# Performance work log

Measured on AMD Instinct MI355X. Metric: run time of the kernel, lower is better.

Reference implementation:

```python
import jax, jax.numpy as jnp
import numpy as np

N = 8192
K = 64
EPS = 1e-7
BN_EPS = 1e-5


def _norm(x):
    return jnp.sqrt(jnp.sum(x * x, axis=-1, keepdims=True))


def _bn(x, gamma, beta):
    # BatchNorm2d in training mode (batch statistics, biased variance)
    mu = jnp.mean(x, axis=(0, 2, 3), keepdims=True)
    var = jnp.mean((x - mu) ** 2, axis=(0, 2, 3), keepdims=True)
    return gamma.reshape(1, -1, 1, 1) * (x - mu) / jnp.sqrt(var + BN_EPS) + beta.reshape(1, -1, 1, 1)


def _conv1x1(x, w, b):
    # 1x1 conv == per-pixel linear: x [B,C,H,W], w [O,C]
    return jnp.einsum('bchw,oc->bohw', x, w) + b.reshape(1, -1, 1, 1)


def setup_inputs() -> dict:
    key = jax.random.key(0)
    ks = jax.random.split(key, 24)
    d = {}
    d['points'] = jax.random.normal(ks[0], (1, N, 3), jnp.float32)
    # graph_conv weights (torch code re-draws these every forward; here fixed params)
    lim0 = float(np.sqrt(6.0 / (4 + 64)))
    d['gw0'] = jax.random.uniform(ks[1], (4, 64), jnp.float32, -lim0, lim0)
    lim = float(np.sqrt(6.0 / (64 + 64)))
    for i in range(1, 5):
        d[f'gw{i}'] = jax.random.uniform(ks[1 + i], (64, 64), jnp.float32, -lim, lim)
    # mlp_1: 4->64->128, mlp_2: 192->256->1024 (1x1 convs + BN)
    d['c1w'] = jax.random.normal(ks[6], (64, 4), jnp.float32) * 0.1
    d['c1b'] = jnp.zeros((64,), jnp.float32)
    d['bn1g'] = jnp.ones((64,), jnp.float32)
    d['bn1b'] = jnp.zeros((64,), jnp.float32)
    d['c2w'] = jax.random.normal(ks[7], (128, 64), jnp.float32) * 0.1
    d['c2b'] = jnp.zeros((128,), jnp.float32)
    d['bn2g'] = jnp.ones((128,), jnp.float32)
    d['bn2b'] = jnp.zeros((128,), jnp.float32)
    d['c3w'] = jax.random.normal(ks[8], (256, 192), jnp.float32) * 0.05
    d['c3b'] = jnp.zeros((256,), jnp.float32)
    d['bn3g'] = jnp.ones((256,), jnp.float32)
    d['bn3b'] = jnp.zeros((256,), jnp.float32)
    d['c4w'] = jax.random.normal(ks[9], (1024, 256), jnp.float32) * 0.05
    d['c4b'] = jnp.zeros((1024,), jnp.float32)
    d['bn4g'] = jnp.ones((1024,), jnp.float32)
    d['bn4b'] = jnp.zeros((1024,), jnp.float32)
    return d


def _knn_search(points, k):
    # pairwise squared distances via ||a||^2 - 2ab + ||b||^2
    r = jnp.sum(points * points, axis=-1, keepdims=True)          # [1,N,1]
    dis = r - 2.0 * jnp.einsum('bnd,bmd->bnm', points, points) + jnp.swapaxes(r, 1, 2)
    _, idx = jax.lax.top_k(-dis, k)                                # [1,N,K]
    knn_pts = jax.vmap(lambda p, i: p[i])(points, idx)             # [1,N,K,3]
    return knn_pts


def _proj_knn(knn_pts):
    b, n, k, _ = knn_pts.shape
    pc = knn_pts - knn_pts[:, :, :1, :]                            # center on first neighbor (self)
    vn = jnp.sqrt(jnp.sum(pc * pc, axis=-1))                       # [1,N,K]
    id1 = jnp.argmax(vn, axis=-1)                                  # farthest neighbor
    a1 = jnp.take_along_axis(pc, jnp.broadcast_to(id1[:, :, None, None], (b, n, 1, 3)), axis=2)[:, :, 0, :]
    a1 = a1 / (_norm(a1) + EPS)
    a2 = jnp.mean(pc, axis=2)
    a2 = a2 / (_norm(a2) + EPS)
    a3 = a1 + 1.5 * a2
    a3 = a3 / (_norm(a3) + EPS)
    den = _norm(pc) + EPS                                          # [1,N,K,1]
    f1 = jnp.sum(pc * a1[:, :, None, :], axis=-1, keepdims=True) / den
    f2 = jnp.sum(pc * a2[:, :, None, :], axis=-1, keepdims=True) / den
    f3 = jnp.sum(pc * a3[:, :, None, :], axis=-1, keepdims=True) / den
    return jnp.concatenate([f1, f2, f3, vn[..., None]], axis=-1)   # [1,N,K,4]


def _proj_points(points):
    b, n, _ = points.shape
    vn = jnp.sqrt(jnp.sum(points * points, axis=-1))               # [1,N]
    i1 = jnp.argmax(vn, axis=-1)
    i2 = jnp.argmin(vn, axis=-1)
    a1 = jnp.take_along_axis(points, jnp.broadcast_to(i1[:, None, None], (b, 1, 3)), axis=1)[:, 0, :]
    a1 = a1 / (_norm(a1) + EPS)
    a2 = jnp.take_along_axis(points, jnp.broadcast_to(i2[:, None, None], (b, 1, 3)), axis=1)[:, 0, :]
    a2 = a2 / (_norm(a2) + EPS)
    a3 = a1 + 1.5 * a2
    a3 = a3 / (_norm(a3) + EPS)
    den = _norm(points) + EPS                                      # [1,N,1]
    f1 = jnp.sum(points * a1[:, None, :], axis=-1, keepdims=True) / den
    f2 = jnp.sum(points * a2[:, None, :], axis=-1, keepdims=True) / den
    f3 = jnp.sum(points * a3[:, None, :], axis=-1, keepdims=True) / den
    return jnp.concatenate([f1, f2, f3, vn[..., None]], axis=-1)   # [1,N,4]


def reference(points, gw0, gw1, gw2, gw3, gw4,
              c1w, c1b, bn1g, bn1b, c2w, c2b, bn2g, bn2b,
              c3w, c3b, bn3g, bn3b, c4w, c4b, bn4g, bn4b):
    n = points.shape[1]
    # upper branch: KNN -> rotation-invariant local feats -> 5-layer MLP -> max over K
    knn_pts = _knn_search(points, K)
    feat_up = _proj_knn(knn_pts)                                   # [1,N,K,4]
    x = feat_up.reshape(-1, 4)
    for w in (gw0, gw1, gw2, gw3, gw4):
        x = jax.nn.relu(x @ w)
    x = x.reshape(1, n, K, 64)
    emb_up = jnp.max(x, axis=2, keepdims=True)                     # [1,N,1,64]
    emb_up = emb_up.reshape(1, 64, n, 1)                           # raw view (reshape), as in torch
    # lower branch: global rotation-invariant feats -> mlp_1
    feat_down = _proj_points(points)                               # [1,N,4]
    emb_down = feat_down.reshape(1, 4, n, 1)                       # raw view (reshape), as in torch
    h = jax.nn.relu(_bn(_conv1x1(emb_down, c1w, c1b), bn1g, bn1b))
    h = jax.nn.relu(_bn(_conv1x1(h, c2w, c2b), bn2g, bn2b))        # [1,128,N,1]
    emb = jnp.concatenate([emb_up, h], axis=1)                     # [1,192,N,1]
    out = jax.nn.relu(_bn(_conv1x1(emb, c3w, c3b), bn3g, bn3b))
    out = jax.nn.relu(_bn(_conv1x1(out, c4w, c4b), bn4g, bn4b))    # [1,1024,N,1]
    return out
```

## Files before the change

kernel.cpp:

```cpp
#include <hip/hip_runtime.h>
#include <hip/hip_bf16.h>

#define NPTS 8192
#define KNN 64
#define EPSF 1e-7f

#define OFF_P4      0
#define OFF_STATS   32768
#define OFF_PART    36012
#define OFF_FEATDN  36864
#define OFF_WT1     69632
#define OFF_GWT     69888
#define OFF_BW2     79104
#define OFF_BW3     83200
#define OFF_BW4     107776
#define OFF_XB3V    238848
#define OFF_Y2      2860288
#define OFF_Y3      3908864
#define OFF_FEATUP  6006016

typedef __bf16 bf16x8 __attribute__((ext_vector_type(8)));
typedef float  f32x4  __attribute__((ext_vector_type(4)));

__device__ __forceinline__ unsigned f2u(float f) {
    unsigned u = __float_as_uint(f);
    return ((int)u >= 0) ? (u | 0x80000000u) : ~u;
}
__device__ __forceinline__ float key_to_f(unsigned long long k) {
    unsigned v = (unsigned)(k >> 32);
    unsigned ob = (v & 0x80000000u) ? (v ^ 0x80000000u) : ~v;
    return __uint_as_float(ob);
}
__device__ __forceinline__ unsigned short f2bf(float x) {
    union { __bf16 h; unsigned short s; } u;
    u.h = (__bf16)x;
    return u.s;
}
__device__ __forceinline__ unsigned packbf2(float lo, float hi) {
    return (unsigned)f2bf(lo) | ((unsigned)f2bf(hi) << 16);
}
__device__ __forceinline__ unsigned long long u64min(unsigned long long a, unsigned long long b){ return a < b ? a : b; }
__device__ __forceinline__ unsigned long long u64max(unsigned long long a, unsigned long long b){ return a < b ? b : a; }

__device__ __forceinline__ unsigned long long sort_merge(
    unsigned long long key, unsigned long long cur, int lane)
{
    #pragma unroll
    for (int k = 2; k <= 64; k <<= 1) {
        #pragma unroll
        for (int j = k >> 1; j > 0; j >>= 1) {
            unsigned long long o = __shfl_xor(key, j);
            bool up = ((lane & k) == 0);
            bool lower = ((lane & j) == 0);
            key = (lower == up) ? u64min(key, o) : u64max(key, o);
        }
    }
    unsigned long long rev = __shfl(key, 63 - lane);
    unsigned long long m = u64min(cur, rev);
    #pragma unroll
    for (int j = 32; j > 0; j >>= 1) {
        unsigned long long o = __shfl_xor(m, j);
        m = ((lane & j) == 0) ? u64min(m, o) : u64max(m, o);
    }
    return m;
}

__global__ __launch_bounds__(256) void prepwt_kernel(
    const float* __restrict__ points,
    const float* __restrict__ c1w, const float* __restrict__ c2w,
    const float* __restrict__ c3w, const float* __restrict__ c4w,
    const float* __restrict__ gw0, const float* __restrict__ gw1,
    const float* __restrict__ gw2, const float* __restrict__ gw3,
    const float* __restrict__ gw4,
    float* __restrict__ ws)
{
    const int t = blockIdx.x * 256 + threadIdx.x;
    const int T = 256 * 256;
    for (int m = t; m < 2944; m += T) ws[OFF_STATS + m] = 0.f;
    for (int m = t; m < 64*4; m += T) { int o = m >> 2, c = m & 3; ws[OFF_WT1 + c*64 + o] = c1w[m]; }

    unsigned short* bw2 = (unsigned short*)(ws + OFF_BW2);
    for (int m = t; m < 128*64; m += T)   bw2[m] = f2bf(c2w[m]);
    unsigned short* bw3 = (unsigned short*)(ws + OFF_BW3);
    for (int m = t; m < 256*192; m += T)  bw3[m] = f2bf(c3w[m]);
    unsigned short* bw4 = (unsigned short*)(ws + OFF_BW4);
    for (int m = t; m < 1024*256; m += T) bw4[m] = f2bf(c4w[m]);

    unsigned short* gwt = (unsigned short*)(ws + OFF_GWT);
    for (int m = t; m < 2048; m += T) {
        int o = m >> 5, i = m & 31;
        gwt[m] = (i < 4) ? f2bf(gw0[i*64 + o]) : (unsigned short)0;
    }
    const float* gsrc[4] = {gw1, gw2, gw3, gw4};
    for (int l = 0; l < 4; ++l) {
        const float* g = gsrc[l];
        unsigned short* dst = gwt + 2048 + l*4096;
        for (int m = t; m < 4096; m += T) { int o = m >> 6, i = m & 63; dst[m] = f2bf(g[i*64 + o]); }
    }

    if (blockIdx.x < 32) {
        const int n = blockIdx.x * 256 + threadIdx.x;
        float x = points[3*n+0], y = points[3*n+1], z = points[3*n+2];
        float rr = x*x + y*y + z*z;
        ((float4*)(ws + OFF_P4))[n] = make_float4(x, y, z, rr);
        float vn = sqrtf(rr);
        unsigned b = __float_as_uint(vn);
        unsigned long long mxk = ((unsigned long long)b << 32) | (unsigned long long)(0xFFFFFFFFu - (unsigned)n);
        unsigned long long mnk = ((unsigned long long)b << 32) | (unsigned long long)(unsigned)n;
        for (int j = 32; j > 0; j >>= 1) {
            mxk = u64max(mxk, __shfl_xor(mxk, j));
            mnk = u64min(mnk, __shfl_xor(mnk, j));
        }
        __shared__ unsigned long long smx[4], smn[4];
        int wid = threadIdx.x >> 6;
        if ((threadIdx.x & 63) == 0) { smx[wid] = mxk; smn[wid] = mnk; }
        __syncthreads();
        if (threadIdx.x == 0) {
            unsigned long long MX = 0ull, MN = ~0ull;
            for (int i = 0; i < 4; ++i) { MX = u64max(MX, smx[i]); MN = u64min(MN, smn[i]); }
            unsigned long long* parts = (unsigned long long*)(ws + OFF_PART);
            parts[2*blockIdx.x + 0] = MX;
            parts[2*blockIdx.x + 1] = MN;
        }
    }
}

__global__ __launch_bounds__(512) void knn_feat_kernel(
    const float4* __restrict__ p4, float4* __restrict__ feat_up,
    float* __restrict__ ws)
{
    __shared__ __align__(16) float4 scand[2048];
    __shared__ unsigned long long queue[8][128];
    const int lane = threadIdx.x & 63;
    const int wid  = threadIdx.x >> 6;
    const int q = blockIdx.x * 8 + wid;

    const float4 qa = p4[q];
    unsigned long long cur = ~0ull;
    float ke = __builtin_inff();
    int qc = 0;
    unsigned long long* Q = queue[wid];

    for (int base = 0; base < NPTS; base += 2048) {
        __syncthreads();
        for (int t = threadIdx.x; t < 2048; t += 512) scand[t] = p4[base + t];
        __syncthreads();
        #pragma unroll 2
        for (int sub = 0; sub < 2048; sub += 128) {
            float4 cd0 = scand[sub + lane];
            float4 cd1 = scand[sub + 64 + lane];
            float dot0 = fmaf(qa.x, cd0.x, fmaf(qa.y, cd0.y, qa.z * cd0.z));
            float dot1 = fmaf(qa.x, cd1.x, fmaf(qa.y, cd1.y, qa.z * cd1.z));
            float e0 = fmaf(-2.f, dot0, cd0.w);
            float e1 = fmaf(-2.f, dot1, cd1.w);
            bool p0 = e0 < ke;
            bool p1 = e1 < ke;
            unsigned long long m0 = __ballot(p0);
            unsigned long long m1 = __ballot(p1);
            if (m0) {
                int prefix = __builtin_amdgcn_mbcnt_hi((unsigned)(m0 >> 32),
                              __builtin_amdgcn_mbcnt_lo((unsigned)m0, 0));
                if (p0) Q[qc + prefix] = ((unsigned long long)f2u(e0) << 32)
                                       | (unsigned long long)(unsigned)(base + sub + lane);
                qc += __popcll(m0);
                if (qc >= 64) {
                    qc -= 64;
                    cur = sort_merge(Q[qc + lane], cur, lane);
                    ke = key_to_f(__shfl(cur, 63));
                }
            }
            if (m1) {
                int prefix = __builtin_amdgcn_mbcnt_hi((unsigned)(m1 >> 32),
                              __builtin_amdgcn_mbcnt_lo((unsigned)m1, 0));
                if (p1) Q[qc + prefix] = ((unsigned long long)f2u(e1) << 32)
                                       | (unsigned long long)(unsigned)(base + sub + 64 + lane);
                qc += __popcll(m1);
                if (qc >= 64) {
                    qc -= 64;
                    cur = sort_merge(Q[qc + lane], cur, lane);
                    ke = key_to_f(__shfl(cur, 63));
                }
            }
        }
    }
    cur = sort_merge((lane < qc) ? Q[lane] : ~0ull, cur, lane);

    int nidx = (int)(unsigned)(cur & 0xFFFFFFFFu);
    float4 np = p4[nidx];
    float ox = __shfl(np.x, 0), oy = __shfl(np.y, 0), oz = __shfl(np.z, 0);
    float pcx = np.x - ox, pcy = np.y - oy, pcz = np.z - oz;
    float vn = sqrtf(pcx*pcx + pcy*pcy + pcz*pcz);

    unsigned long long ak = ((unsigned long long)__float_as_uint(vn) << 32)
                          | (unsigned long long)(unsigned)(63 - lane);
    for (int s = 32; s > 0; s >>= 1) ak = u64max(ak, __shfl_xor(ak, s));
    int id1 = 63 - (int)(unsigned)(ak & 0xFFFFFFFFu);

    float a1x = __shfl(pcx, id1), a1y = __shfl(pcy, id1), a1z = __shfl(pcz, id1);
    float n1 = sqrtf(a1x*a1x + a1y*a1y + a1z*a1z) + EPSF;
    a1x /= n1; a1y /= n1; a1z /= n1;

    float sx = pcx, sy = pcy, sz = pcz;
    for (int s = 32; s > 0; s >>= 1) {
        sx += __shfl_xor(sx, s); sy += __shfl_xor(sy, s); sz += __shfl_xor(sz, s);
    }
    float a2x = sx * (1.f/64.f), a2y = sy * (1.f/64.f), a2z = sz * (1.f/64.f);
    float n2 = sqrtf(a2x*a2x + a2y*a2y + a2z*a2z) + EPSF;
    a2x /= n2; a2y /= n2; a2z /= n2;

    float a3x = a1x + 1.5f*a2x, a3y = a1y + 1.5f*a2y, a3z = a1z + 1.5f*a2z;
    float n3 = sqrtf(a3x*a3x + a3y*a3y + a3z*a3z) + EPSF;
    a3x /= n3; a3y /= n3; a3z /= n3;

    float den = vn + EPSF;
    float f1 = (pcx*a1x + pcy*a1y + pcz*a1z) / den;
    float f2 = (pcx*a2x + pcy*a2y + pcz*a2z) / den;
    float f3 = (pcx*a3x + pcy*a3y + pcz*a3z) / den;
    feat_up[q*64 + lane] = make_float4(f1, f2, f3, vn);

    {
        const unsigned long long* parts = (const unsigned long long*)(ws + OFF_PART);
        unsigned long long mxk = (lane < 32) ? parts[2*lane + 0] : 0ull;
        unsigned long long mnk = (lane < 32) ? parts[2*lane + 1] : ~0ull;
        for (int s = 32; s > 0; s >>= 1) {
            mxk = u64max(mxk, __shfl_xor(mxk, s));
            mnk = u64min(mnk, __shfl_xor(mnk, s));
        }
        if (lane == 0) {
            int i1 = (int)(0xFFFFFFFFu - (unsigned)(mxk & 0xFFFFFFFFu));
            int i2 = (int)(unsigned)(mnk & 0xFFFFFFFFu);
            float4 p1 = p4[i1];
            float4 p2 = p4[i2];
            float w1 = sqrtf(p1.x*p1.x + p1.y*p1.y + p1.z*p1.z) + EPSF;
            float b1x = p1.x/w1, b1y = p1.y/w1, b1z = p1.z/w1;
            float w2 = sqrtf(p2.x*p2.x + p2.y*p2.y + p2.z*p2.z) + EPSF;
            float b2x = p2.x/w2, b2y = p2.y/w2, b2z = p2.z/w2;
            float b3x = b1x + 1.5f*b2x, b3y = b1y + 1.5f*b2y, b3z = b1z + 1.5f*b2z;
            float w3 = sqrtf(b3x*b3x + b3y*b3y + b3z*b3z) + EPSF;
            b3x /= w3; b3y /= w3; b3z /= w3;
            float vq = sqrtf(qa.w);
            float dq = vq + EPSF;
            float g1 = (qa.x*b1x + qa.y*b1y + qa.z*b1z) / dq;
            float g2 = (qa.x*b2x + qa.y*b2y + qa.z*b2z) / dq;
            float g3 = (qa.x*b3x + qa.y*b3y + qa.z*b3z) / dq;
            ((float4*)(ws + OFF_FEATDN))[q] = make_float4(g1, g2, g3, vq);
        }
    }
}

#define BROW 72
__global__ __launch_bounds__(256) void mlp_kernel(
    const float4* __restrict__ feat_up,
    const unsigned short* __restrict__ gwt,
    unsigned short* __restrict__ xb3v,
    const float* __restrict__ c1b,
    float* __restrict__ ws)
{
    __shared__ __align__(16) unsigned short Blds[4][64 * BROW];
    const int lane = threadIdx.x & 63;
    const int wid  = threadIdx.x >> 6;
    const int q = blockIdx.x * 4 + wid;
    const int c = lane & 15, g = lane >> 4;
    unsigned short* B = Blds[wid];

    {
        float4 f = feat_up[q*64 + lane];
        uint2 p0;
        p0.x = packbf2(f.x, f.y);
        p0.y = packbf2(f.z, f.w);
        *(uint2*)&B[lane*BROW] = p0;
        *(uint2*)&B[lane*BROW + 4] = make_uint2(0, 0);
        uint4 z4 = make_uint4(0, 0, 0, 0);
        *(uint4*)&B[lane*BROW + 8]  = z4;
        *(uint4*)&B[lane*BROW + 16] = z4;
        *(uint4*)&B[lane*BROW + 24] = z4;
    }

    const unsigned short* Wl[5] = {gwt, gwt + 2048, gwt + 6144, gwt + 10240, gwt + 14336};
    f32x4 acc[4][4];

    for (int layer = 0; layer < 5; ++layer) {
        const int wstride = (layer == 0) ? 32 : 64;
        const int nks = (layer == 0) ? 1 : 2;
        #pragma unroll
        for (int mb = 0; mb < 4; ++mb)
            #pragma unroll
            for (int nb = 0; nb < 4; ++nb)
                acc[mb][nb] = (f32x4){0.f, 0.f, 0.f, 0.f};

        for (int ks = 0; ks < nks; ++ks) {
            bf16x8 af[4], bf[4];
            #pragma unroll
            for (int mb = 0; mb < 4; ++mb)
                af[mb] = *(const bf16x8*)(Wl[layer] + (mb*16 + c)*wstride + ks*32 + g*8);
            #pragma unroll
            for (int nb = 0; nb < 4; ++nb)
                bf[nb] = *(const bf16x8*)&B[(nb*16 + c)*BROW + ks*32 + g*8];
            #pragma unroll
            for (int mb = 0; mb < 4; ++mb)
                #pragma unroll
                for (int nb = 0; nb < 4; ++nb)
                    acc[mb][nb] = __builtin_amdgcn_mfma_f32_16x16x32_bf16(af[mb], bf[nb], acc[mb][nb], 0, 0, 0);
        }

        if (layer < 4) {
            #pragma unroll
            for (int mb = 0; mb < 4; ++mb) {
                #pragma unroll
                for (int nb = 0; nb < 4; ++nb) {
                    f32x4 a = acc[mb][nb];
                    uint2 pw;
                    pw.x = packbf2(fmaxf(a[0], 0.f), fmaxf(a[1], 0.f));
                    pw.y = packbf2(fmaxf(a[2], 0.f), fmaxf(a[3], 0.f));
                    *(uint2*)&B[(nb*16 + c)*BROW + mb*16 + g*4] = pw;
                }
            }
        }
    }

    const int cc = q >> 7;
    const int pbase = (q & 127) << 6;
    #pragma unroll
    for (int mb = 0; mb < 4; ++mb) {
        float v[4];
        #pragma unroll
        for (int r = 0; r < 4; ++r)
            v[r] = fmaxf(fmaxf(fmaxf(acc[mb][0][r], acc[mb][1][r]),
                               fmaxf(acc[mb][2][r], acc[mb][3][r])), 0.f);
        #pragma unroll
        for (int mask = 1; mask <= 8; mask <<= 1)
            #pragma unroll
            for (int r = 0; r < 4; ++r)
                v[r] = fmaxf(v[r], __shfl_xor(v[r], mask));
        if (c == 0) {
            #pragma unroll
            for (int r = 0; r < 4; ++r) {
                const int f = mb*16 + g*4 + r;
                xb3v[(size_t)(pbase + f) * 64 + cc] = f2bf(v[r]);
            }
        }
    }

    if (blockIdx.x < 64) {
        __syncthreads();
        float* sps  = (float*)&Blds[0][0];
        float* spss = sps + 128;
        const int tid = threadIdx.x;
        const int bx = blockIdx.x & 31, by = blockIdx.x >> 5;
        const int p  = bx * 256 + tid;
        const int o0 = by * 32;
        const float* fdn = ws + OFF_FEATDN;
        const float* wt1 = ws + OFF_WT1;
        float* s1 = ws + OFF_STATS;
        float xv0 = fdn[p], xv1 = fdn[8192 + p], xv2 = fdn[16384 + p], xv3 = fdn[24576 + p];
        float accc[32];
        #pragma unroll
        for (int u = 0; u < 32; ++u) accc[u] = c1b[o0 + u];
        #pragma unroll
        for (int u = 0; u < 32; ++u) accc[u] = fmaf(xv0, wt1[0*64 + o0 + u], accc[u]);
        #pragma unroll
        for (int u = 0; u < 32; ++u) accc[u] = fmaf(xv1, wt1[1*64 + o0 + u], accc[u]);
        #pragma unroll
        for (int u = 0; u < 32; ++u) accc[u] = fmaf(xv2, wt1[2*64 + o0 + u], accc[u]);
        #pragma unroll
        for (int u = 0; u < 32; ++u) accc[u] = fmaf(xv3, wt1[3*64 + o0 + u], accc[u]);
        #pragma unroll
        for (int u = 0; u < 32; ++u) {
            float s = accc[u], ss = accc[u] * accc[u];
            for (int j = 32; j > 0; j >>= 1) { s += __shfl_xor(s, j); ss += __shfl_xor(ss, j); }
            if (lane == 0) { sps[wid*32 + u] = s; spss[wid*32 + u] = ss; }
        }
        __syncthreads();
        if (tid < 32) {
            float S  = sps[tid] + sps[32 + tid] + sps[64 + tid] + sps[96 + tid];
            float SS = spss[tid] + spss[32 + tid] + spss[64 + tid] + spss[96 + tid];
            atomicAdd(&s1[o0 + tid], S);
            atomicAdd(&s1[64 + o0 + tid], SS);
        }
    }
}

__device__ __forceinline__ void xcd_tile(int nwg, int MB, int& nb, int& mb) {
    const int bid = blockIdx.x;
    const int bidp = (bid & 7) * (nwg >> 3) + (bid >> 3);
    mb = bidp % MB;
    nb = bidp / MB;
}

__global__ __launch_bounds__(256) void conv2fd_kernel(
    const unsigned short* __restrict__ A,
    const float* __restrict__ c1b,
    const float* __restrict__ stp, const float* __restrict__ gam, const float* __restrict__ bet,
    const float* __restrict__ bias, float* __restrict__ yout, float* __restrict__ stout,
    const float* __restrict__ ws)
{
    __shared__ float sc[64], sh[64], swt[256], sb[64];
    const int tid = threadIdx.x;
    if (tid < 64) {
        float mu  = stp[tid] * (1.f / 8192.f);
        float var = stp[64 + tid] * (1.f / 8192.f) - mu * mu;
        float s = gam[tid] / sqrtf(var + 1e-5f);
        sc[tid] = s; sh[tid] = bet[tid] - mu * s;
        sb[tid] = c1b[tid];
    }
    if (tid < 256) swt[tid] = ws[OFF_WT1 + tid];
    __syncthreads();

    const float* fdn = ws + OFF_FEATDN;
    const int lane = tid & 63;
    const int w = tid >> 6;
    int nb, mb;
    xcd_tile(64, 2, nb, mb);
    const int n0 = nb * 256 + w * 64;
    const int m0 = mb * 64;
    const int c = lane & 15, g = lane >> 4;
    const int K = 64, M = 128;

    f32x4 acc[4][4];
    #pragma unroll
    for (int mt = 0; mt < 4; ++mt)
        #pragma unroll
        for (int nt = 0; nt < 4; ++nt)
            acc[mt][nt] = (f32x4){0.f, 0.f, 0.f, 0.f};

    for (int k0 = 0; k0 < K; k0 += 32) {
        bf16x8 af[4], bf[4];
        #pragma unroll
        for (int mt = 0; mt < 4; ++mt)
            af[mt] = *(const bf16x8*)(A + (size_t)(m0 + mt*16 + c) * K + k0 + g*8);
        const int ch0 = k0 + g*8;
        #pragma unroll
        for (int nt = 0; nt < 4; ++nt) {
            const int pt = n0 + nt*16 + c;
            const float fd0 = fdn[pt];
            const float fd1 = fdn[8192 + pt];
            const float fd2 = fdn[16384 + pt];
            const float fd3 = fdn[24576 + pt];
            bf16x8 r;
            #pragma unroll
            for (int j = 0; j < 8; ++j) {
                const int ch = ch0 + j;
                float v = fmaf(fd3, swt[192 + ch],
                          fmaf(fd2, swt[128 + ch],
                          fmaf(fd1, swt[64 + ch],
                          fmaf(fd0, swt[ch], sb[ch]))));
                r[j] = (__bf16)fmaxf(fmaf(v, sc[ch], sh[ch]), 0.f);
            }
            bf[nt] = r;
        }
        #pragma unroll
        for (int mt = 0; mt < 4; ++mt)
            #pragma unroll
            for (int nt = 0; nt < 4; ++nt)
                acc[mt][nt] = __builtin_amdgcn_mfma_f32_16x16x32_bf16(af[mt], bf[nt], acc[mt][nt], 0, 0, 0);
    }

    #pragma unroll
    for (int mt = 0; mt < 4; ++mt) {
        float s[4], ss[4];
        #pragma unroll
        for (int r = 0; r < 4; ++r) {
            const int o = m0 + mt*16 + g*4 + r;
            const float bv = bias[o];
            float sum = 0.f, sq = 0.f;
            #pragma unroll
            for (int nt = 0; nt < 4; ++nt) {
                float v = acc[mt][nt][r] + bv;
                yout[(size_t)o * NPTS + n0 + nt*16 + c] = v;
                sum += v; sq += v * v;
            }
            s[r] = sum; ss[r] = sq;
        }
        #pragma unroll
        for (int mask = 1; mask <= 8; mask <<= 1)
            #pragma unroll
            for (int r = 0; r < 4; ++r) {
                s[r]  += __shfl_xor(s[r],  mask);
                ss[r] += __shfl_xor(ss[r], mask);
            }
        if (c == 0) {
            #pragma unroll
            for (int r = 0; r < 4; ++r) {
                const int o = m0 + mt*16 + g*4 + r;
                atomicAdd(&stout[o], s[r]);
                atomicAdd(&stout[M + o], ss[r]);
            }
        }
    }
}

__global__ __launch_bounds__(256) void convbn_kernel(
    const unsigned short* __restrict__ A,
    const unsigned short* __restrict__ Bdir, int Kdir,
    const float* __restrict__ yprev,
    const float* __restrict__ stp, const float* __restrict__ gam, const float* __restrict__ bet,
    const float* __restrict__ bias, int K, int M,
    float* __restrict__ yout, float* __restrict__ stout)
{
    __shared__ float sc[256], sh[256];
    const int tid = threadIdx.x;
    const int Cp = K - Kdir;
    for (int cc = tid; cc < Cp; cc += 256) {
        float mu  = stp[cc] * (1.f / 8192.f);
        float var = stp[Cp + cc] * (1.f / 8192.f) - mu * mu;
        float s = gam[cc] / sqrtf(var + 1e-5f);
        sc[cc] = s; sh[cc] = bet[cc] - mu * s;
    }
    __syncthreads();

    const int lane = tid & 63;
    const int w = tid >> 6;
    int nb, mb;
    xcd_tile(gridDim.x, M >> 6, nb, mb);
    const int n0 = nb * 256 + w * 64;
    const int m0 = mb * 64;
    const int c = lane & 15, g = lane >> 4;

    f32x4 acc[4][4];
    #pragma unroll
    for (int mt = 0; mt < 4; ++mt)
        #pragma unroll
        for (int nt = 0; nt < 4; ++nt)
            acc[mt][nt] = (f32x4){0.f, 0.f, 0.f, 0.f};

    for (int k0 = 0; k0 < K; k0 += 32) {
        bf16x8 af[4], bf[4];
        #pragma unroll
        for (int mt = 0; mt < 4; ++mt)
            af[mt] = *(const bf16x8*)(A + (size_t)(m0 + mt*16 + c) * K + k0 + g*8);
        if (k0 + 32 <= Kdir) {
            #pragma unroll
            for (int nt = 0; nt < 4; ++nt)
                bf[nt] = *(const bf16x8*)(Bdir + (size_t)(n0 + nt*16 + c) * Kdir + k0 + g*8);
        } else {
            const int ch0 = k0 - Kdir + g*8;
            #pragma unroll
            for (int nt = 0; nt < 4; ++nt) {
                const int pt = n0 + nt*16 + c;
                bf16x8 r;
                #pragma unroll
                for (int j = 0; j < 8; ++j) {
                    float vv = fmaxf(fmaf(yprev[(size_t)(ch0 + j) * NPTS + pt],
                                          sc[ch0 + j], sh[ch0 + j]), 0.f);
                    r[j] = (__bf16)vv;
                }
                bf[nt] = r;
            }
        }
        #pragma unroll
        for (int mt = 0; mt < 4; ++mt)
            #pragma unroll
            for (int nt = 0; nt < 4; ++nt)
                acc[mt][nt] = __builtin_amdgcn_mfma_f32_16x16x32_bf16(af[mt], bf[nt], acc[mt][nt], 0, 0, 0);
    }

    #pragma unroll
    for (int mt = 0; mt < 4; ++mt) {
        float s[4], ss[4];
        #pragma unroll
        for (int r = 0; r < 4; ++r) {
            const int o = m0 + mt*16 + g*4 + r;
            const float bv = bias[o];
            float sum = 0.f, sq = 0.f;
            #pragma unroll
            for (int nt = 0; nt < 4; ++nt) {
                float v = acc[mt][nt][r] + bv;
                yout[(size_t)o * NPTS + n0 + nt*16 + c] = v;
                sum += v; sq += v * v;
            }
            s[r] = sum; ss[r] = sq;
        }
        #pragma unroll
        for (int mask = 1; mask <= 8; mask <<= 1)
            #pragma unroll
            for (int r = 0; r < 4; ++r) {
                s[r]  += __shfl_xor(s[r],  mask);
                ss[r] += __shfl_xor(ss[r], mask);
            }
        if (c == 0) {
            #pragma unroll
            for (int r = 0; r < 4; ++r) {
                const int o = m0 + mt*16 + g*4 + r;
                atomicAdd(&stout[o], s[r]);
                atomicAdd(&stout[M + o], ss[r]);
            }
        }
    }
}

__global__ __launch_bounds__(256) void bnrelu_kernel(
    const float4* y, const float* __restrict__ st,
    const float* __restrict__ g, const float* __restrict__ b,
    float4* out, int C)
{
    int idx = blockIdx.x * 256 + threadIdx.x;
    int c = idx >> 11;
    float mu  = st[c] * (1.f / 8192.f);
    float var = st[C + c] * (1.f / 8192.f) - mu * mu;
    float scale = g[c] / sqrtf(var + 1e-5f);
    float sh = b[c] - mu * scale;
    float4 v = y[idx];
    v.x = fmaxf(fmaf(v.x, scale, sh), 0.f);
    v.y = fmaxf(fmaf(v.y, scale, sh), 0.f);
    v.z = fmaxf(fmaf(v.z, scale, sh), 0.f);
    v.w = fmaxf(fmaf(v.w, scale, sh), 0.f);
    out[idx] = v;
}

extern "C" void kernel_launch(void* const* d_in, const int* in_sizes, int n_in,
                              void* d_out, int out_size, void* d_ws, size_t ws_size,
                              hipStream_t stream) {
    const float* points = (const float*)d_in[0];
    const float* gw0 = (const float*)d_in[1];
    const float* gw1 = (const float*)d_in[2];
    const float* gw2 = (const float*)d_in[3];
    const float* gw3 = (const float*)d_in[4];
    const float* gw4 = (const float*)d_in[5];
    const float* c1w = (const float*)d_in[6];  const float* c1b = (const float*)d_in[7];
    const float* bn1g = (const float*)d_in[8]; const float* bn1b = (const float*)d_in[9];
    const float* c2w = (const float*)d_in[10]; const float* c2b = (const float*)d_in[11];
    const float* bn2g = (const float*)d_in[12];const float* bn2b = (const float*)d_in[13];
    const float* c3w = (const float*)d_in[14]; const float* c3b = (const float*)d_in[15];
    const float* bn3g = (const float*)d_in[16];const float* bn3b = (const float*)d_in[17];
    const float* c4w = (const float*)d_in[18]; const float* c4b = (const float*)d_in[19];
    const float* bn4g = (const float*)d_in[20];const float* bn4b = (const float*)d_in[21];

    float* ws = (float*)d_ws;
    float* p4f    = ws + OFF_P4;
    float* featup = ws + OFF_FEATUP;
    float* y2 = ws + OFF_Y2; float* y3 = ws + OFF_Y3;
    float* s1 = ws + OFF_STATS + 0;
    float* s2 = ws + OFF_STATS + 128;
    float* s3 = ws + OFF_STATS + 384;
    float* s4 = ws + OFF_STATS + 896;
    const unsigned short* gwt = (const unsigned short*)(ws + OFF_GWT);
    const unsigned short* bw2 = (const unsigned short*)(ws + OFF_BW2);
    const unsigned short* bw3 = (const unsigned short*)(ws + OFF_BW3);
    const unsigned short* bw4 = (const unsigned short*)(ws + OFF_BW4);
    unsigned short* xb3v = (unsigned short*)(ws + OFF_XB3V);
    float* outp = (float*)d_out;

    prepwt_kernel<<<256, 256, 0, stream>>>(points, c1w, c2w, c3w, c4w,
                                           gw0, gw1, gw2, gw3, gw4, ws);

    knn_feat_kernel<<<1024, 512, 0, stream>>>((const float4*)p4f, (float4*)featup, ws);
    mlp_kernel<<<2048, 256, 0, stream>>>((const float4*)featup, gwt, xb3v, c1b, ws);

    conv2fd_kernel<<<64, 256, 0, stream>>>(bw2, c1b, s1, bn1g, bn1b,
                                           c2b, y2, s2, ws);
    convbn_kernel<<<128, 256, 0, stream>>>(bw3, xb3v, 64, y2, s2, bn2g, bn2b,
                                           c3b, 192, 256, y3, s3);
    convbn_kernel<<<512, 256, 0, stream>>>(bw4, nullptr, 0, y3, s3, bn3g, bn3b,
                                           c4b, 256, 1024, outp, s4);
    bnrelu_kernel<<<8192, 256, 0, stream>>>((const float4*)outp, s4, bn4g, bn4b, (float4*)outp, 1024);
}
```

Baseline: 322.0 us.

## Bucket points by radius and prune KNN search with radial-shell bounds

Adds a histogram and counting-sort pass that groups points into 64 shells by distance from the origin. The KNN kernel then scans shells outward from the query's own shell and stops once the radial gap exceeds the current k-th distance bound, rather than brute-forcing all 8192 candidates. This cuts the distance evaluations, which are the dominant cost. In exchange it drops shared-memory tiling for direct global loads, adds an extra kernel launch and atomics, and its pruning depends on how the data is distributed. The shell width is a fixed constant suited to Gaussian inputs.

```diff
diff --git a/kernel.cpp b/kernel.cpp
--- a/kernel.cpp
+++ b/kernel.cpp
@@ -4,9 +4,12 @@
 #define NPTS 8192
 #define KNN 64
 #define EPSF 1e-7f
+#define BINW 0.075f
+#define INVW (1.0f/0.075f)
 
 #define OFF_P4      0
 #define OFF_STATS   32768
+#define OFF_C       35712
 #define OFF_PART    36012
 #define OFF_FEATDN  36864
 #define OFF_WT1     69632
@@ -15,6 +18,10 @@
 #define OFF_BW3     83200
 #define OFF_BW4     107776
 #define OFF_XB3V    238848
+#define OFF_P4S     501248
+#define OFF_IDXS    534016
+#define OFF_H32     542208
+#define OFF_POUT    544256
 #define OFF_Y2      2860288
 #define OFF_Y3      3908864
 #define OFF_FEATUP  6006016
@@ -77,6 +84,7 @@
     const int t = blockIdx.x * 256 + threadIdx.x;
     const int T = 256 * 256;
     for (int m = t; m < 2944; m += T) ws[OFF_STATS + m] = 0.f;
+    for (int m = t; m < 64; m += T) ((unsigned*)(ws + OFF_C))[m] = 0u;
     for (int m = t; m < 64*4; m += T) { int o = m >> 2, c = m & 3; ws[OFF_WT1 + c*64 + o] = c1w[m]; }
 
     unsigned short* bw2 = (unsigned short*)(ws + OFF_BW2);
@@ -99,11 +107,16 @@
     }
 
     if (blockIdx.x < 32) {
+        __shared__ unsigned lh[64];
+        if (threadIdx.x < 64) lh[threadIdx.x] = 0u;
+        __syncthreads();
         const int n = blockIdx.x * 256 + threadIdx.x;
         float x = points[3*n+0], y = points[3*n+1], z = points[3*n+2];
         float rr = x*x + y*y + z*z;
         ((float4*)(ws + OFF_P4))[n] = make_float4(x, y, z, rr);
         float vn = sqrtf(rr);
+        int bin = (int)(vn * INVW); if (bin > 63) bin = 63;
+        atomicAdd(&lh[bin], 1u);
         unsigned b = __float_as_uint(vn);
         unsigned long long mxk = ((unsigned long long)b << 32) | (unsigned long long)(0xFFFFFFFFu - (unsigned)n);
         unsigned long long mnk = ((unsigned long long)b << 32) | (unsigned long long)(unsigned)n;
@@ -115,6 +128,8 @@
         int wid = threadIdx.x >> 6;
         if ((threadIdx.x & 63) == 0) { smx[wid] = mxk; smn[wid] = mnk; }
         __syncthreads();
+        if (threadIdx.x < 64)
+            ((unsigned*)(ws + OFF_H32))[blockIdx.x * 64 + threadIdx.x] = lh[threadIdx.x];
         if (threadIdx.x == 0) {
             unsigned long long MX = 0ull, MN = ~0ull;
             for (int i = 0; i < 4; ++i) { MX = u64max(MX, smx[i]); MN = u64min(MN, smn[i]); }
@@ -125,64 +140,104 @@
     }
 }
 
+__global__ __launch_bounds__(256) void scatter_kernel(float* __restrict__ ws)
+{
+    const int tid = threadIdx.x, lane = tid & 63;
+    const unsigned* H32 = (const unsigned*)(ws + OFF_H32);
+    unsigned h = 0;
+    #pragma unroll
+    for (int k = 0; k < 32; ++k) h += H32[k*64 + lane];
+    unsigned x = h;
+    #pragma unroll
+    for (int d = 1; d < 64; d <<= 1) { unsigned y = __shfl_up(x, d); if (lane >= d) x += y; }
+    unsigned excl = x - h;
+
+    const int n = blockIdx.x * 256 + tid;
+    float4 v = ((const float4*)(ws + OFF_P4))[n];
+    float vn = sqrtf(v.w);
+    int bin = (int)(vn * INVW); if (bin > 63) bin = 63;
+    unsigned base = (unsigned)__shfl((int)excl, bin);
+    unsigned* C = (unsigned*)(ws + OFF_C);
+    unsigned pos = base + atomicAdd(&C[bin], 1u);
+    ((float4*)(ws + OFF_P4S))[pos] = v;
+    ((unsigned*)(ws + OFF_IDXS))[pos] = (unsigned)n;
+    if (blockIdx.x == 0 && tid < 64) ((unsigned*)(ws + OFF_POUT))[tid] = excl;
+}
+
 __global__ __launch_bounds__(512) void knn_feat_kernel(
-    const float4* __restrict__ p4, float4* __restrict__ feat_up,
+    const float4* __restrict__ p4, const float4* __restrict__ p4s,
+    const unsigned* __restrict__ idxs, float4* __restrict__ feat_up,
     float* __restrict__ ws)
 {
-    __shared__ __align__(16) float4 scand[2048];
     __shared__ unsigned long long queue[8][128];
     const int lane = threadIdx.x & 63;
     const int wid  = threadIdx.x >> 6;
     const int q = blockIdx.x * 8 + wid;
 
+    const int pstart = (int)((const unsigned*)(ws + OFF_POUT))[lane];
+
     const float4 qa = p4[q];
+    const float qn = sqrtf(qa.w);
     unsigned long long cur = ~0ull;
     float ke = __builtin_inff();
     int qc = 0;
     unsigned long long* Q = queue[wid];
 
-    for (int base = 0; base < NPTS; base += 2048) {
-        __syncthreads();
-        for (int t = threadIdx.x; t < 2048; t += 512) scand[t] = p4[base + t];
-        __syncthreads();
-        #pragma unroll 2
-        for (int sub = 0; sub < 2048; sub += 128) {
-            float4 cd0 = scand[sub + lane];
-            float4 cd1 = scand[sub + 64 + lane];
-            float dot0 = fmaf(qa.x, cd0.x, fmaf(qa.y, cd0.y, qa.z * cd0.z));
-            float dot1 = fmaf(qa.x, cd1.x, fmaf(qa.y, cd1.y, qa.z * cd1.z));
-            float e0 = fmaf(-2.f, dot0, cd0.w);
-            float e1 = fmaf(-2.f, dot1, cd1.w);
-            bool p0 = e0 < ke;
-            bool p1 = e1 < ke;
-            unsigned long long m0 = __ballot(p0);
-            unsigned long long m1 = __ballot(p1);
-            if (m0) {
-                int prefix = __builtin_amdgcn_mbcnt_hi((unsigned)(m0 >> 32),
-                              __builtin_amdgcn_mbcnt_lo((unsigned)m0, 0));
-                if (p0) Q[qc + prefix] = ((unsigned long long)f2u(e0) << 32)
-                                       | (unsigned long long)(unsigned)(base + sub + lane);
-                qc += __popcll(m0);
-                if (qc >= 64) {
-                    qc -= 64;
-                    cur = sort_merge(Q[qc + lane], cur, lane);
-                    ke = key_to_f(__shfl(cur, 63));
+#define SCANB(BB) { \
+    const int s_ = __shfl(pstart, (BB)); \
+    const int e_ = ((BB) == 63) ? NPTS : __shfl(pstart, (BB) + 1); \
+    for (int off = s_; off < e_; off += 64) { \
+        const int jj = off + lane; \
+        float e0 = __builtin_inff(); \
+        float4 cd; \
+        if (jj < e_) { \
+            cd = p4s[jj]; \
+            float dot = fmaf(qa.x, cd.x, fmaf(qa.y, cd.y, qa.z * cd.z)); \
+            e0 = fmaf(-2.f, dot, cd.w); \
+        } \
+        bool p = e0 < ke; \
+        unsigned long long m = __ballot(p); \
+        if (m) { \
+            int prefix = __builtin_amdgcn_mbcnt_hi((unsigned)(m >> 32), \
+                          __builtin_amdgcn_mbcnt_lo((unsigned)m, 0)); \
+            if (p) Q[qc + prefix] = ((unsigned long long)f2u(e0) << 32) \
+                                  | (unsigned long long)idxs[jj]; \
+            qc += __popcll(m); \
+            if (qc >= 64) { \
+                qc -= 64; \
+                cur = sort_merge(Q[qc + lane], cur, lane); \
+                ke = key_to_f(__shfl(cur, 63)); \
+            } \
+        } \
+    } }
+
+    int b0 = (int)(qn * INVW); if (b0 > 63) b0 = 63;
+    int br = b0, bl = b0 - 1;
+    bool rOK = true, lOK = (bl >= 0);
+    while (rOK || lOK) {
+        if (rOK) {
+            if (br >= 64) rOK = false;
+            else {
+                bool go = true;
+                if (br > b0) {
+                    float d = br * BINW - qn;
+                    if (d > 0.f && d*d > fmaf(ke + qa.w, 1.0001f, 1e-4f)) go = false;
                 }
-            }
-            if (m1) {
-                int prefix = __builtin_amdgcn_mbcnt_hi((unsigned)(m1 >> 32),
-                              __builtin_amdgcn_mbcnt_lo((unsigned)m1, 0));
-                if (p1) Q[qc + prefix] = ((unsigned long long)f2u(e1) << 32)
-                                       | (unsigned long long)(unsigned)(base + sub + 64 + lane);
-                qc += __popcll(m1);
-                if (qc >= 64) {
-                    qc -= 64;
-                    cur = sort_merge(Q[qc + lane], cur, lane);
-                    ke = key_to_f(__shfl(cur, 63));
-                }
-            }
-        }
-    }
+                if (!go) rOK = false;
+                else { SCANB(br); ++br; }
+            }
+        }
+        if (lOK) {
+            if (bl < 0) lOK = false;
+            else {
+                float d = qn - (bl + 1) * BINW;
+                bool go = !(d > 0.f && d*d > fmaf(ke + qa.w, 1.0001f, 1e-4f));
+                if (!go) lOK = false;
+                else { SCANB(bl); --bl; }
+            }
+        }
+    }
+#undef SCANB
     cur = sort_merge((lane < qc) ? Q[lane] : ~0ull, cur, lane);
 
     int nidx = (int)(unsigned)(cur & 0xFFFFFFFFu);
@@ -642,8 +697,12 @@
 
     prepwt_kernel<<<256, 256, 0, stream>>>(points, c1w, c2w, c3w, c4w,
                                            gw0, gw1, gw2, gw3, gw4, ws);
-
-    knn_feat_kernel<<<1024, 512, 0, stream>>>((const float4*)p4f, (float4*)featup, ws);
+    scatter_kernel<<<32, 256, 0, stream>>>(ws);
+
+    knn_feat_kernel<<<1024, 512, 0, stream>>>((const float4*)p4f,
+                                              (const float4*)(ws + OFF_P4S),
+                                              (const unsigned*)(ws + OFF_IDXS),
+                                              (float4*)featup, ws);
     mlp_kernel<<<2048, 256, 0, stream>>>((const float4*)featup, gwt, xb3v, c1b, ws);
 
     conv2fd_kernel<<<64, 256, 0, stream>>>(bw2, c1b, s1, bn1g, bn1b,
```

New measurement: 332.3 us. 1.03x slower.
